# Optimization experiments

Hardware: AMD Instinct MI355X
Metric: run time of the kernel (lower is better)

Reference implementation:

```python
import jax, jax.numpy as jnp
import numpy as np

D_MODEL = 256; N_HEADS = 8; D_FFN = 1024; N_LEVELS = 4; N_POINTS = 4
HEAD_DIM = D_MODEL // N_HEADS
SHAPES = ((100, 100), (50, 50), (25, 25), (13, 13))  # static (H, W) per level
LEN_V = sum(h * w for h, w in SHAPES)  # 13294
BS = 8; NQ = 900


def layer_norm(x, g, b, eps=1e-5):
    m = x.mean(-1, keepdims=True)
    v = ((x - m) ** 2).mean(-1, keepdims=True)
    return (x - m) * jax.lax.rsqrt(v + eps) * g + b


def bilinear_sample(val, loc, H, W):
    # val: [bs, nH, H*W, hd]; loc: [bs, nq, nH, P, 2] normalized to [0,1].
    # Matches torch grid_sample(bilinear, zeros padding, align_corners=False)
    # with grid = 2*loc - 1, i.e. pixel coords x = loc_x*W - 0.5.
    bs, nq, nH, P, _ = loc.shape
    x = loc[..., 0] * W - 0.5
    y = loc[..., 1] * H - 0.5
    x0 = jnp.floor(x); y0 = jnp.floor(y)
    fx = x - x0; fy = y - y0  # grads flow to loc through fx/fy
    x0 = x0.astype(jnp.int32); y0 = y0.astype(jnp.int32)
    out = jnp.zeros((bs, nq, nH, P, HEAD_DIM), val.dtype)
    for dy, wy in ((0, 1.0 - fy), (1, fy)):
        for dx, wx in ((0, 1.0 - fx), (1, fx)):
            xi = x0 + dx; yi = y0 + dy
            valid = (xi >= 0) & (xi < W) & (yi >= 0) & (yi < H)
            idx = jnp.clip(yi, 0, H - 1) * W + jnp.clip(xi, 0, W - 1)  # [bs,nq,nH,P]
            idx = idx.transpose(0, 2, 1, 3).reshape(bs, nH, nq * P)
            g = jnp.take_along_axis(val, idx[..., None], axis=2)  # [bs,nH,nq*P,hd]
            g = g.reshape(bs, nH, nq, P, HEAD_DIM).transpose(0, 2, 1, 3, 4)
            w = (wx * wy * valid).astype(val.dtype)[..., None]
            out = out + g * w
    return out  # [bs, nq, nH, P, hd]


def setup_inputs() -> dict:
    key = jax.random.key(0)
    ks = jax.random.split(key, 16)
    d = D_MODEL
    w = lambda k, shape: (jax.random.normal(k, shape) * 0.02).astype(jnp.float32)
    z = lambda n: jnp.zeros((n,), jnp.float32)
    o = lambda n: jnp.ones((n,), jnp.float32)
    return {
        "embed": jax.random.normal(ks[0], (BS, NQ, d), jnp.float32),
        "refer_bbox": jax.random.uniform(ks[1], (BS, NQ, 4), jnp.float32),  # cxcywh in [0,1]
        "feats": jax.random.normal(ks[2], (BS, LEN_V, d), jnp.float32),
        "query_pos": jax.random.normal(ks[3], (BS, NQ, d), jnp.float32),
        "Wq": w(ks[4], (d, d)), "bq": z(d), "Wk": w(ks[5], (d, d)), "bk": z(d),
        "Wv": w(ks[6], (d, d)), "bv": z(d), "Wo": w(ks[7], (d, d)), "bo": z(d),
        "g1": o(d), "b1": z(d),
        "Wval": w(ks[8], (d, d)), "bval": z(d),
        "Woff": w(ks[9], (d, N_HEADS * N_LEVELS * N_POINTS * 2)), "boff": z(N_HEADS * N_LEVELS * N_POINTS * 2),
        "Waw": w(ks[10], (d, N_HEADS * N_LEVELS * N_POINTS)), "baw": z(N_HEADS * N_LEVELS * N_POINTS),
        "Wop": w(ks[11], (d, d)), "bop": z(d),
        "g2": o(d), "b2": z(d),
        "W1": w(ks[12], (d, D_FFN)), "bf1": z(D_FFN),
        "W2": w(ks[13], (D_FFN, d)), "bf2": z(d),
        "g3": o(d), "b3": z(d),
    }


def reference(embed, refer_bbox, feats, query_pos, Wq, bq, Wk, bk, Wv, bv, Wo, bo,
              g1, b1, Wval, bval, Woff, boff, Waw, baw, Wop, bop, g2, b2,
              W1, bf1, W2, bf2, g3, b3):
    bs, nq, d = embed.shape
    # ---- self attention (q = k = embed + query_pos, v = embed) ----
    qk_in = embed + query_pos
    q = (qk_in @ Wq + bq).reshape(bs, nq, N_HEADS, HEAD_DIM)
    k = (qk_in @ Wk + bk).reshape(bs, nq, N_HEADS, HEAD_DIM)
    v = (embed @ Wv + bv).reshape(bs, nq, N_HEADS, HEAD_DIM)
    scores = jnp.einsum('bqhd,bkhd->bhqk', q, k) * (HEAD_DIM ** -0.5)
    attn = jax.nn.softmax(scores, -1)
    sa = jnp.einsum('bhqk,bkhd->bqhd', attn, v).reshape(bs, nq, d) @ Wo + bo
    embed = layer_norm(embed + sa, g1, b1)
    # ---- MSDeformAttn cross attention ----
    query = embed + query_pos
    rb = refer_bbox[:, :, None, :]  # [bs, nq, 1, 4] (refer_bbox.unsqueeze(2))
    value = (feats @ Wval + bval).reshape(bs, LEN_V, N_HEADS, HEAD_DIM)
    off = (query @ Woff + boff).reshape(bs, nq, N_HEADS, N_LEVELS, N_POINTS, 2)
    aw = jax.nn.softmax((query @ Waw + baw).reshape(bs, nq, N_HEADS, N_LEVELS * N_POINTS), -1)
    aw = aw.reshape(bs, nq, N_HEADS, N_LEVELS, N_POINTS)
    # num_points == 4 branch: loc = cxcy + off/P * wh * 0.5
    loc = rb[:, :, None, :, None, :2] + off / N_POINTS * rb[:, :, None, :, None, 2:] * 0.5
    out = jnp.zeros((bs, nq, N_HEADS, HEAD_DIM), embed.dtype)
    start = 0
    for l, (H, W) in enumerate(SHAPES):
        val_l = value[:, start:start + H * W].transpose(0, 2, 1, 3)  # [bs,nH,HW,hd]
        s = bilinear_sample(val_l, loc[:, :, :, l], H, W)  # [bs,nq,nH,P,hd]
        out = out + (s * aw[:, :, :, l, :, None]).sum(3)
        start += H * W
    ca = out.reshape(bs, nq, d) @ Wop + bop
    embed = layer_norm(embed + ca, g2, b2)
    # ---- FFN ----
    ff = jax.nn.relu(embed @ W1 + bf1) @ W2 + bf2
    return layer_norm(embed + ff, g3, b3)
```

## Files before the change

### kernel.cpp

```cpp
#include <hip/hip_runtime.h>
#include <hip/hip_bf16.h>
#include <cstddef>

#define BS 8
#define NQ 900
#define DM 256
#define LEN_V 13294

using bf16x8 = __attribute__((ext_vector_type(8))) __bf16;
using f32x4  = __attribute__((ext_vector_type(4))) float;

__device__ __forceinline__ unsigned short f2bf(float f) {
    union { float f; unsigned int u; } v; v.f = f;
    unsigned int r = v.u + 0x7FFFu + ((v.u >> 16) & 1u);
    return (unsigned short)(r >> 16);
}
__device__ __forceinline__ float bf2f(unsigned short u) {
    union { unsigned int u; float f; } v; v.u = ((unsigned int)u) << 16;
    return v.f;
}

#define SW(r) (((r) + ((r) >> 2)) & 3)

#define FLAG_RELU 1
#define FLAG_OBF  2
#define FLAG_SWAP 4
#define FLAG_QKV  8

#define AS1(p) ((const __attribute__((address_space(1))) void*)(p))
#define AS3(p) ((__attribute__((address_space(3))) void*)(p))

#define DRAIN_DMA() do {                                   \
    __builtin_amdgcn_sched_barrier(0);                     \
    asm volatile("s_waitcnt vmcnt(0)" ::: "memory");       \
    __builtin_amdgcn_sched_barrier(0);                     \
} while (0)

struct WDesc { const float* src; unsigned short* dst; int K; int N; float scale; };
struct WPrepArgs { WDesc w[10]; };

__global__ __launch_bounds__(256) void wprep_kernel(WPrepArgs args)
{
    WDesc d = args.w[blockIdx.z];
    int k0 = blockIdx.x * 32;
    int n0 = blockIdx.y * 32;
    if (k0 >= d.K || n0 >= d.N) return;
    __shared__ unsigned short t[32][33];
    int tx = threadIdx.x & 31, ty = threadIdx.x >> 5;
    #pragma unroll
    for (int i = 0; i < 4; ++i) {
        int kk = ty + i * 8;
        t[kk][tx] = f2bf(d.src[(size_t)(k0 + kk) * d.N + n0 + tx] * d.scale);
    }
    __syncthreads();
    #pragma unroll
    for (int i = 0; i < 4; ++i) {
        int nn = ty + i * 8;
        d.dst[(size_t)(n0 + nn) * d.K + k0 + tx] = t[tx][nn];
    }
}

__global__ __launch_bounds__(256) void bias_concat_kernel(
    const float* __restrict__ bq, const float* __restrict__ bk,
    const float* __restrict__ bv, const float* __restrict__ boff,
    const float* __restrict__ baw, float* __restrict__ bqkv,
    float* __restrict__ boffaw)
{
    const float sc = 0.17677669529663687f;
    int t = blockIdx.x * 256 + threadIdx.x;
    if (t < 256)       bqkv[t] = bq[t] * sc;
    else if (t < 512)  bqkv[t] = bk[t - 256];
    else if (t < 768)  bqkv[t] = bv[t - 512];
    if (t < 256)       boffaw[t] = boff[t];
    else if (t < 384)  boffaw[t] = baw[t - 256];
}

__global__ __launch_bounds__(256) void gemm_val(
    const float* __restrict__ A, const unsigned short* __restrict__ BT,
    const float* __restrict__ bias, unsigned short* __restrict__ C,
    int M, int N, int K)
{
    __shared__ uint4 SMEM[3072];

    const int tid = threadIdx.x;
    const int lane = tid & 63;
    const int wave = tid >> 6;
    const int wm = wave >> 1;
    const int wn = wave & 1;
    const int row0 = blockIdx.y * 128;
    const int col0 = blockIdx.x * 128;

    f32x4 acc[4][4];
    #pragma unroll
    for (int i = 0; i < 4; ++i)
        #pragma unroll
        for (int j = 0; j < 4; ++j)
            acc[i][j] = {0.f, 0.f, 0.f, 0.f};

    const int lr = lane & 15;
    const int lc = lane >> 4;

    const int achunk = (lane & 7) ^ ((lane >> 3) & 7);
    const int bchunk = (lane & 3) ^ ((lane >> 2) & 3);

    auto STAGE = [&](int k0, int buf) {
        uint4* Ab = SMEM + buf * 1536;
        uint4* Bb = Ab + 1024;
        #pragma unroll
        for (int c = 0; c < 4; ++c) {
            int r = wave * 32 + c * 8 + (lane >> 3);
            int gr = row0 + r; if (gr >= M) gr = M - 1;
            const float* g = A + (size_t)gr * K + k0 + achunk * 4;
            __builtin_amdgcn_global_load_lds(AS1(g), AS3(Ab + (wave * 4 + c) * 64), 16, 0, 0);
        }
        #pragma unroll
        for (int c = 0; c < 2; ++c) {
            int r = wave * 32 + c * 16 + (lane >> 2);
            const unsigned short* g = BT + (size_t)(col0 + r) * K + k0 + bchunk * 8;
            __builtin_amdgcn_global_load_lds(AS1(g), AS3(Bb + (wave * 2 + c) * 64), 16, 0, 0);
        }
    };

    auto MSTEP = [&](int buf) {
        const float* Af = (const float*)(SMEM + buf * 1536);
        const bf16x8* Bb8 = (const bf16x8*)(SMEM + buf * 1536 + 1024);
        bf16x8 af[4], bfr[4];
        #pragma unroll
        for (int mi = 0; mi < 4; ++mi) {
            int R = wm * 64 + mi * 16 + lr;
            int s0 = (2 * lc) ^ (R & 7);
            int s1 = (2 * lc + 1) ^ (R & 7);
            f32x4 a0 = *(const f32x4*)(Af + R * 32 + s0 * 4);
            f32x4 a1 = *(const f32x4*)(Af + R * 32 + s1 * 4);
            union { unsigned short us[8]; bf16x8 v; } u;
            u.us[0] = f2bf(a0[0]); u.us[1] = f2bf(a0[1]);
            u.us[2] = f2bf(a0[2]); u.us[3] = f2bf(a0[3]);
            u.us[4] = f2bf(a1[0]); u.us[5] = f2bf(a1[1]);
            u.us[6] = f2bf(a1[2]); u.us[7] = f2bf(a1[3]);
            af[mi] = u.v;
        }
        #pragma unroll
        for (int ni = 0; ni < 4; ++ni) {
            int R = wn * 64 + ni * 16 + lr;
            bfr[ni] = Bb8[R * 4 + (lc ^ (R & 3))];
        }
        #pragma unroll
        for (int mi = 0; mi < 4; ++mi)
            #pragma unroll
            for (int ni = 0; ni < 4; ++ni)
                acc[mi][ni] = __builtin_amdgcn_mfma_f32_16x16x32_bf16(
                    af[mi], bfr[ni], acc[mi][ni], 0, 0, 0);
    };

    const int NS = K >> 5;
    STAGE(0, 0);
    DRAIN_DMA();
    __syncthreads();
    for (int s = 0; s < NS; s += 2) {
        if (s + 1 < NS) STAGE((s + 1) * 32, 1);
        MSTEP(0);
        DRAIN_DMA();
        __syncthreads();
        if (s + 2 < NS) STAGE((s + 2) * 32, 0);
        MSTEP(1);
        DRAIN_DMA();
        __syncthreads();
    }

    {
        unsigned short* RP = (unsigned short*)SMEM;
        float bval[4];
        #pragma unroll
        for (int ni = 0; ni < 4; ++ni) {
            int col = col0 + wn * 64 + ni * 16 + lr;
            bval[ni] = (col < N) ? bias[col] : 0.f;
        }
        #pragma unroll
        for (int h2 = 0; h2 < 2; ++h2) {
            __syncthreads();
            if (wm == h2) {
                #pragma unroll
                for (int ni = 0; ni < 4; ++ni) {
                    int colL = wn * 64 + ni * 16 + lr;
                    #pragma unroll
                    for (int mi = 0; mi < 4; ++mi) {
                        #pragma unroll
                        for (int rg = 0; rg < 4; ++rg) {
                            int rowL = mi * 16 + lc * 4 + rg;
                            RP[rowL * 136 + colL] = f2bf(acc[mi][ni][rg] + bval[ni]);
                        }
                    }
                }
            }
            __syncthreads();
            {
                int r = tid >> 2;
                int c = tid & 3;
                int grow = row0 + h2 * 64 + r;
                if (grow < M) {
                    #pragma unroll
                    for (int j = 0; j < 4; ++j) {
                        int gcol = col0 + c * 32 + j * 8;
                        uint4 vq = *(const uint4*)&RP[r * 136 + c * 32 + j * 8];
                        *(uint4*)(C + (size_t)grow * N + gcol) = vq;
                    }
                }
            }
        }
    }
}

#define SLOADA(B, k0) do {                                                    \
    if constexpr (ABF) {                                                      \
        const unsigned short* ap_ = Abf + (size_t)agr * K + (k0) + ah;        \
        qa##B = aok ? *(const uint4*)ap_ : z4;                                \
    } else {                                                                  \
        if (aok) {                                                            \
            const float* ap_ = Afp + (size_t)agr * K + (k0) + ah;             \
            pa##B##0 = *(const f32x4*)(ap_);                                  \
            pa##B##1 = *(const f32x4*)(ap_ + 4);                              \
            if (A2) {                                                         \
                const float* a2_ = A2 + (size_t)agr * K + (k0) + ah;          \
                pa##B##0 += *(const f32x4*)(a2_);                             \
                pa##B##1 += *(const f32x4*)(a2_ + 4);                         \
            }                                                                 \
        } else { pa##B##0 = zf4; pa##B##1 = zf4; }                            \
    }                                                                         \
    { const unsigned short* bp_ = BT + (size_t)bgr * K + (k0) + ah;           \
      pb##B = *(const uint4*)bp_; }                                           \
} while (0)

#define SSTAGE(B) do {                                                        \
    if constexpr (ABF) {                                                      \
        As4[ar * 4 + (ac ^ SW(ar))] = qa##B;                                  \
    } else {                                                                  \
        union { unsigned short us_[8]; uint4 q_; } u_;                        \
        u_.us_[0] = f2bf(pa##B##0[0]); u_.us_[1] = f2bf(pa##B##0[1]);         \
        u_.us_[2] = f2bf(pa##B##0[2]); u_.us_[3] = f2bf(pa##B##0[3]);         \
        u_.us_[4] = f2bf(pa##B##1[0]); u_.us_[5] = f2bf(pa##B##1[1]);         \
        u_.us_[6] = f2bf(pa##B##1[2]); u_.us_[7] = f2bf(pa##B##1[3]);         \
        As4[ar * 4 + (ac ^ SW(ar))] = u_.q_;                                  \
    }                                                                         \
    Bs4[ar * 4 + (ac ^ SW(ar))] = pb##B;                                      \
} while (0)

#define SMFMA() do {                                                          \
    bf16x8 af[2], bfr[2];                                                     \
    _Pragma("unroll")                                                         \
    for (int mi = 0; mi < 2; ++mi) {                                          \
        int r = wm * 32 + mi * 16 + lr;                                       \
        af[mi] = Asb[r * 4 + (lc ^ SW(r))];                                   \
    }                                                                         \
    _Pragma("unroll")                                                         \
    for (int ni = 0; ni < 2; ++ni) {                                          \
        int r = wn * 32 + ni * 16 + lr;                                       \
        bfr[ni] = Bsb[r * 4 + (lc ^ SW(r))];                                  \
    }                                                                         \
    _Pragma("unroll")                                                         \
    for (int mi = 0; mi < 2; ++mi)                                            \
        _Pragma("unroll")                                                     \
        for (int ni = 0; ni < 2; ++ni)                                        \
            acc[mi][ni] = __builtin_amdgcn_mfma_f32_16x16x32_bf16(            \
                af[mi], bfr[ni], acc[mi][ni], 0, 0, 0);                       \
} while (0)

template<int ABF>
__global__ __launch_bounds__(256) void gemm_small(
    const void* __restrict__ Ain, const float* __restrict__ A2,
    const unsigned short* __restrict__ BT, const float* __restrict__ bias,
    void* __restrict__ Cout, int M, int N, int K, int flags)
{
    __shared__ uint4 SMEM[512];
    uint4* As4 = SMEM;
    uint4* Bs4 = SMEM + 256;

    const int tid = threadIdx.x;
    const int lane = tid & 63;
    const int wave = tid >> 6;
    const int wm = wave >> 1;
    const int wn = wave & 1;
    const int row0 = (flags & FLAG_SWAP ? blockIdx.y : blockIdx.x) * 64;
    const int col0 = (flags & FLAG_SWAP ? blockIdx.x : blockIdx.y) * 64;
    if ((flags & FLAG_QKV) && col0 >= 512) A2 = nullptr;

    const float* Afp = (const float*)Ain;
    const unsigned short* Abf = (const unsigned short*)Ain;

    f32x4 acc[2][2];
    #pragma unroll
    for (int i = 0; i < 2; ++i)
        #pragma unroll
        for (int j = 0; j < 2; ++j)
            acc[i][j] = {0.f, 0.f, 0.f, 0.f};

    const int ar = tid >> 2;
    const int ac = tid & 3;
    const int ah = ac * 8;
    const int agr = row0 + ar;
    const bool aok = agr < M;
    const int bgr = col0 + ar;
    const int lr = lane & 15;
    const int lc = lane >> 4;

    const bf16x8* Asb = (const bf16x8*)As4;
    const bf16x8* Bsb = (const bf16x8*)Bs4;
    const uint4 z4 = {0u, 0u, 0u, 0u};
    const f32x4 zf4 = {0.f, 0.f, 0.f, 0.f};

    f32x4 pa00, pa01, pa10, pa11;
    uint4 qa0, qa1;
    uint4 pb0, pb1;

    const int nsteps = K >> 5;
    SLOADA(0, 0);
    for (int s = 0; s < nsteps; s += 2) {
        __syncthreads();
        SSTAGE(0);
        SLOADA(1, (s + 1 < nsteps ? (s + 1) * 32 : 0));
        __syncthreads();
        SMFMA();
        __syncthreads();
        SSTAGE(1);
        SLOADA(0, (s + 2 < nsteps ? (s + 2) * 32 : 0));
        __syncthreads();
        SMFMA();
    }

    const int relu = flags & FLAG_RELU;
    if (!(flags & FLAG_OBF)) {
        float* C = (float*)Cout;
        #pragma unroll
        for (int ni = 0; ni < 2; ++ni) {
            int col = col0 + wn * 32 + ni * 16 + lr;
            if (col >= N) continue;
            float bval = bias[col];
            #pragma unroll
            for (int mi = 0; mi < 2; ++mi) {
                #pragma unroll
                for (int rg = 0; rg < 4; ++rg) {
                    int row = row0 + wm * 32 + mi * 16 + lc * 4 + rg;
                    if (row < M) {
                        float o = acc[mi][ni][rg] + bval;
                        if (relu) o = fmaxf(o, 0.f);
                        C[(size_t)row * N + col] = o;
                    }
                }
            }
        }
    } else {
        unsigned short* RP = (unsigned short*)SMEM;
        unsigned short* C = (unsigned short*)Cout;
        float bval[2];
        #pragma unroll
        for (int ni = 0; ni < 2; ++ni) {
            int col = col0 + wn * 32 + ni * 16 + lr;
            bval[ni] = (col < N) ? bias[col] : 0.f;
        }
        #pragma unroll
        for (int h2 = 0; h2 < 2; ++h2) {
            __syncthreads();
            if (wm == h2) {
                #pragma unroll
                for (int ni = 0; ni < 2; ++ni) {
                    int colL = wn * 32 + ni * 16 + lr;
                    #pragma unroll
                    for (int mi = 0; mi < 2; ++mi) {
                        #pragma unroll
                        for (int rg = 0; rg < 4; ++rg) {
                            int rowL = mi * 16 + lc * 4 + rg;
                            float o = acc[mi][ni][rg] + bval[ni];
                            if (relu) o = fmaxf(o, 0.f);
                            RP[rowL * 72 + colL] = f2bf(o);
                        }
                    }
                }
            }
            __syncthreads();
            {
                int r = tid >> 3;
                int c = tid & 7;
                int grow = row0 + h2 * 32 + r;
                int gcol = col0 + c * 8;
                if (grow < M && gcol < N) {
                    uint4 vq = *(const uint4*)&RP[r * 72 + c * 8];
                    *(uint4*)(C + (size_t)grow * N + gcol) = vq;
                }
            }
        }
    }
}

#define QKVS 768
__global__ __launch_bounds__(256) void attn_mfma_kernel(
    const unsigned short* __restrict__ qkv, float* __restrict__ out)
{
    __shared__ uint4 Kls[64 * 4];
    __shared__ uint4 Vtls[32 * 8];

    const int tid = threadIdx.x;
    const int lane = tid & 63;
    const int wave = tid >> 6;
    const int qcol = lane & 15;
    const int g = lane >> 4;
    const int bh = blockIdx.x;
    const int h = bh & 7, b = bh >> 3;
    const int qg = blockIdx.y * 64 + wave * 16 + qcol;
    const int qc = qg < NQ ? qg : NQ - 1;

    bf16x8 qf = *(const bf16x8*)(qkv + ((size_t)(b * NQ + qc)) * QKVS + h * 32 + g * 8);

    float mrun = -3.0e38f, lrun = 0.f;
    f32x4 oacc[2];
    oacc[0] = {0.f, 0.f, 0.f, 0.f};
    oacc[1] = {0.f, 0.f, 0.f, 0.f};
    const f32x4 zacc = {0.f, 0.f, 0.f, 0.f};

    const int kidx = tid >> 2, kdc = tid & 3;
    const int vkp = tid >> 3, vdc = tid & 7;
    const bf16x8* Kb = (const bf16x8*)Kls;
    const bf16x8* Vb = (const bf16x8*)Vtls;
    unsigned int* V32 = (unsigned int*)Vtls;

    for (int jb = 0; jb < NQ; jb += 64) {
        __syncthreads();
        {
            int gk = jb + kidx;
            const uint4 z = {0u, 0u, 0u, 0u};
            uint4 kv = (gk < NQ)
                ? *(const uint4*)(qkv + ((size_t)(b * NQ + gk)) * QKVS + 256 + h * 32 + kdc * 8)
                : z;
            Kls[kidx * 4 + (kdc ^ ((kidx >> 1) & 3))] = kv;
        }
        {
            int k0g = jb + 2 * vkp;
            ushort4 a = {0, 0, 0, 0}, c = {0, 0, 0, 0};
            if (k0g < NQ)
                a = *(const ushort4*)(qkv + ((size_t)(b * NQ + k0g)) * QKVS + 512 + h * 32 + vdc * 4);
            if (k0g + 1 < NQ)
                c = *(const ushort4*)(qkv + ((size_t)(b * NQ + k0g + 1)) * QKVS + 512 + h * 32 + vdc * 4);
            unsigned int p0 = (unsigned int)a.x | ((unsigned int)c.x << 16);
            unsigned int p1 = (unsigned int)a.y | ((unsigned int)c.y << 16);
            unsigned int p2 = (unsigned int)a.z | ((unsigned int)c.z << 16);
            unsigned int p3 = (unsigned int)a.w | ((unsigned int)c.w << 16);
            int d0 = vdc * 4;
            V32[(d0+0) * 32 + ((vkp >> 2) ^ ((d0+0) & 7)) * 4 + (vkp & 3)] = p0;
            V32[(d0+1) * 32 + ((vkp >> 2) ^ ((d0+1) & 7)) * 4 + (vkp & 3)] = p1;
            V32[(d0+2) * 32 + ((vkp >> 2) ^ ((d0+2) & 7)) * 4 + (vkp & 3)] = p2;
            V32[(d0+3) * 32 + ((vkp >> 2) ^ ((d0+3) & 7)) * 4 + (vkp & 3)] = p3;
        }
        __syncthreads();

        f32x4 sacc[4];
        #pragma unroll
        for (int kt = 0; kt < 4; ++kt) {
            int key = kt * 16 + qcol;
            bf16x8 kf = Kb[key * 4 + (g ^ ((key >> 1) & 3))];
            sacc[kt] = __builtin_amdgcn_mfma_f32_16x16x32_bf16(kf, qf, zacc, 0, 0, 0);
        }
        if (jb + 64 > NQ) {
            #pragma unroll
            for (int kt = 0; kt < 4; ++kt)
                #pragma unroll
                for (int r = 0; r < 4; ++r)
                    if (jb + kt * 16 + 4 * g + r >= NQ) sacc[kt][r] = -3.0e38f;
        }

        float mloc = -3.0e38f;
        #pragma unroll
        for (int kt = 0; kt < 4; ++kt)
            #pragma unroll
            for (int r = 0; r < 4; ++r)
                mloc = fmaxf(mloc, sacc[kt][r]);
        mloc = fmaxf(mloc, __shfl_xor(mloc, 16));
        mloc = fmaxf(mloc, __shfl_xor(mloc, 32));
        float mnew = fmaxf(mrun, mloc);
        float corr = __expf(mrun - mnew);
        mrun = mnew;

        float lloc = 0.f;
        unsigned int pk2[4][2];
        #pragma unroll
        for (int kt = 0; kt < 4; ++kt) {
            float p0 = __expf(sacc[kt][0] - mnew);
            float p1 = __expf(sacc[kt][1] - mnew);
            float p2 = __expf(sacc[kt][2] - mnew);
            float p3 = __expf(sacc[kt][3] - mnew);
            lloc += p0 + p1 + p2 + p3;
            pk2[kt][0] = (unsigned int)f2bf(p0) | ((unsigned int)f2bf(p1) << 16);
            pk2[kt][1] = (unsigned int)f2bf(p2) | ((unsigned int)f2bf(p3) << 16);
        }
        lloc += __shfl_xor(lloc, 16);
        lloc += __shfl_xor(lloc, 32);
        lrun = lrun * corr + lloc;
        #pragma unroll
        for (int ni = 0; ni < 2; ++ni)
            #pragma unroll
            for (int r = 0; r < 4; ++r)
                oacc[ni][r] *= corr;

        const int s0 = qcol + 32 * (g & 1);
        const bool hi = (g >> 1) != 0;
        #pragma unroll
        for (int tp = 0; tp < 2; ++tp) {
            int A0 = (int)pk2[2 * tp][0], A1 = (int)pk2[2 * tp][1];
            int B0 = (int)pk2[2 * tp + 1][0], B1 = (int)pk2[2 * tp + 1][1];
            int a0 = __shfl(A0, s0),      a1 = __shfl(A1, s0);
            int b0 = __shfl(B0, s0),      b1 = __shfl(B1, s0);
            int a2 = __shfl(A0, s0 + 16), a3 = __shfl(A1, s0 + 16);
            int b2 = __shfl(B0, s0 + 16), b3 = __shfl(B1, s0 + 16);
            union { unsigned int u[4]; bf16x8 v8; } pf;
            pf.u[0] = hi ? (unsigned int)b0 : (unsigned int)a0;
            pf.u[1] = hi ? (unsigned int)b1 : (unsigned int)a1;
            pf.u[2] = hi ? (unsigned int)b2 : (unsigned int)a2;
            pf.u[3] = hi ? (unsigned int)b3 : (unsigned int)a3;
            #pragma unroll
            for (int ni = 0; ni < 2; ++ni) {
                int d = ni * 16 + qcol;
                bf16x8 vf = Vb[d * 8 + ((4 * tp + g) ^ (d & 7))];
                oacc[ni] = __builtin_amdgcn_mfma_f32_16x16x32_bf16(vf, pf.v8, oacc[ni], 0, 0, 0);
            }
        }
    }

    if (qg < NQ) {
        float inv = 1.f / lrun;
        float* op = out + ((size_t)(b * NQ + qg)) * DM + h * 32;
        float4 o0, o1;
        o0.x = oacc[0][0] * inv; o0.y = oacc[0][1] * inv;
        o0.z = oacc[0][2] * inv; o0.w = oacc[0][3] * inv;
        o1.x = oacc[1][0] * inv; o1.y = oacc[1][1] * inv;
        o1.z = oacc[1][2] * inv; o1.w = oacc[1][3] * inv;
        *(float4*)(op + 4 * g) = o0;
        *(float4*)(op + 16 + 4 * g) = o1;
    }
}

__global__ __launch_bounds__(256) void aw_softmax_kernel(float* __restrict__ offaw)
{
    int t = blockIdx.x * 256 + threadIdx.x;
    if (t >= BS * NQ * 8) return;
    int row = t >> 3, h = t & 7;
    float* p = offaw + (size_t)row * 384 + 256 + h * 16;
    float vals[16];
    #pragma unroll
    for (int i = 0; i < 4; ++i) {
        float4 f = *(const float4*)(p + i * 4);
        vals[4 * i + 0] = f.x; vals[4 * i + 1] = f.y;
        vals[4 * i + 2] = f.z; vals[4 * i + 3] = f.w;
    }
    float mx = vals[0];
    #pragma unroll
    for (int i = 1; i < 16; ++i) mx = fmaxf(mx, vals[i]);
    float sum = 0.f;
    #pragma unroll
    for (int i = 0; i < 16; ++i) { vals[i] = __expf(vals[i] - mx); sum += vals[i]; }
    float inv = 1.f / sum;
    #pragma unroll
    for (int i = 0; i < 4; ++i) {
        float4 f;
        f.x = vals[4 * i + 0] * inv; f.y = vals[4 * i + 1] * inv;
        f.z = vals[4 * i + 2] * inv; f.w = vals[4 * i + 3] * inv;
        *(float4*)(p + i * 4) = f;
    }
}

__global__ __launch_bounds__(256) void deform_kernel(
    const unsigned short* __restrict__ value, const float* __restrict__ offaw,
    const float* __restrict__ rbbox, float* __restrict__ dout)
{
    int t = blockIdx.x * 256 + threadIdx.x;
    if (t >= BS * NQ * 64) return;
    int c = t & 7;
    int h = (t >> 3) & 7;
    int bq = t >> 6;
    int b = bq / NQ;

    const int Hs[4]     = {100, 50, 25, 13};
    const int Wsz[4]    = {100, 50, 25, 13};
    const int Starts[4] = {0, 10000, 12500, 13125};

    float4 rb = *(const float4*)(rbbox + (size_t)bq * 4);
    const float* offp = offaw + (size_t)bq * 384 + h * 32;
    const float* awp  = offaw + (size_t)bq * 384 + 256 + h * 16;
    const unsigned short* vb = value + ((size_t)b * LEN_V) * 256 + h * 32 + c * 4;

    float4 acc = make_float4(0.f, 0.f, 0.f, 0.f);
    #pragma unroll
    for (int l = 0; l < 4; ++l) {
        const int H = Hs[l], W = Wsz[l], st = Starts[l];
        #pragma unroll
        for (int p = 0; p < 4; ++p) {
            float ox = offp[l * 8 + p * 2 + 0];
            float oy = offp[l * 8 + p * 2 + 1];
            float a_w = awp[l * 4 + p];
            float xx = (rb.x + ox * 0.125f * rb.z) * W - 0.5f;
            float yy = (rb.y + oy * 0.125f * rb.w) * H - 0.5f;
            float x0f = floorf(xx), y0f = floorf(yy);
            float fx = xx - x0f, fy = yy - y0f;
            int x0 = (int)x0f, y0 = (int)y0f;
            #pragma unroll
            for (int dy = 0; dy < 2; ++dy) {
                int yi = y0 + dy;
                float wy = dy ? fy : (1.f - fy);
                bool vy = (yi >= 0) && (yi < H);
                int yc = min(max(yi, 0), H - 1);
                #pragma unroll
                for (int dx = 0; dx < 2; ++dx) {
                    int xi = x0 + dx;
                    float wx = dx ? fx : (1.f - fx);
                    bool vx = (xi >= 0) && (xi < W);
                    int xc = min(max(xi, 0), W - 1);
                    float wgt = a_w * wy * wx * ((vx && vy) ? 1.f : 0.f);
                    ushort4 gv = *(const ushort4*)(vb + (size_t)(st + yc * W + xc) * 256);
                    acc.x += wgt * bf2f(gv.x); acc.y += wgt * bf2f(gv.y);
                    acc.z += wgt * bf2f(gv.z); acc.w += wgt * bf2f(gv.w);
                }
            }
        }
    }
    *(float4*)(dout + (size_t)bq * 256 + h * 32 + c * 4) = acc;
}

__global__ __launch_bounds__(256) void ln_kernel(
    const float* __restrict__ x, const float* __restrict__ dx,
    const float* __restrict__ g, const float* __restrict__ bt,
    float* __restrict__ out, int rows)
{
    int row = blockIdx.x * 4 + (threadIdx.x >> 6);
    if (row >= rows) return;
    int lane = threadIdx.x & 63;
    size_t base = (size_t)row * 256 + lane * 4;
    float4 xv = *(const float4*)(x + base);
    float4 dv = *(const float4*)(dx + base);
    float a0 = xv.x + dv.x, a1 = xv.y + dv.y, a2 = xv.z + dv.z, a3 = xv.w + dv.w;
    float s = a0 + a1 + a2 + a3;
    float s2 = a0 * a0 + a1 * a1 + a2 * a2 + a3 * a3;
    #pragma unroll
    for (int o = 32; o; o >>= 1) {
        s += __shfl_xor(s, o);
        s2 += __shfl_xor(s2, o);
    }
    float mean = s * (1.f / 256.f);
    float var = s2 * (1.f / 256.f) - mean * mean;
    float inv = rsqrtf(var + 1e-5f);
    float4 gv = *(const float4*)(g + lane * 4);
    float4 bv = *(const float4*)(bt + lane * 4);
    float4 r;
    r.x = (a0 - mean) * inv * gv.x + bv.x;
    r.y = (a1 - mean) * inv * gv.y + bv.y;
    r.z = (a2 - mean) * inv * gv.z + bv.z;
    r.w = (a3 - mean) * inv * gv.w + bv.w;
    *(float4*)(out + base) = r;
}

extern "C" void kernel_launch(void* const* d_in, const int* in_sizes, int n_in,
                              void* d_out, int out_size, void* d_ws, size_t ws_size,
                              hipStream_t stream)
{
    const float* embed = (const float*)d_in[0];
    const float* rbbox = (const float*)d_in[1];
    const float* feats = (const float*)d_in[2];
    const float* qpos  = (const float*)d_in[3];
    const float* Wq = (const float*)d_in[4];  const float* bq = (const float*)d_in[5];
    const float* Wk = (const float*)d_in[6];  const float* bk = (const float*)d_in[7];
    const float* Wv = (const float*)d_in[8];  const float* bv = (const float*)d_in[9];
    const float* Wo = (const float*)d_in[10]; const float* bo = (const float*)d_in[11];
    const float* g1 = (const float*)d_in[12]; const float* b1 = (const float*)d_in[13];
    const float* Wval = (const float*)d_in[14]; const float* bval = (const float*)d_in[15];
    const float* Woff = (const float*)d_in[16]; const float* boff = (const float*)d_in[17];
    const float* Waw  = (const float*)d_in[18]; const float* baw  = (const float*)d_in[19];
    const float* Wop  = (const float*)d_in[20]; const float* bop  = (const float*)d_in[21];
    const float* g2 = (const float*)d_in[22]; const float* b2 = (const float*)d_in[23];
    const float* W1 = (const float*)d_in[24]; const float* bf1 = (const float*)d_in[25];
    const float* W2 = (const float*)d_in[26]; const float* bf2 = (const float*)d_in[27];
    const float* g3 = (const float*)d_in[28]; const float* b3 = (const float*)d_in[29];

    const int M = BS * NQ;
    const int MV = BS * LEN_V;
    const size_t E = (size_t)M * DM;
    const size_t VAL = (size_t)MV * DM;

    float* ws = (float*)d_ws;
    float* valueb = ws;
    float* qkvreg = ws + VAL;
    float* attb   = qkvreg + 3 * E;
    float* e1b    = attb + E;
    unsigned short* wbase = (unsigned short*)(e1b + E);
    unsigned short* wqkv_t   = wbase;
    unsigned short* wo_t     = wbase + 196608;
    unsigned short* wval_t   = wbase + 262144;
    unsigned short* woffaw_t = wbase + 327680;
    unsigned short* wop_t    = wbase + 425984;
    unsigned short* w1_t     = wbase + 491520;
    unsigned short* w2_t     = wbase + 753664;
    float* bqkv   = (float*)(wbase + 1015808);
    float* boffaw = bqkv + 768;

    unsigned short* valuebf = (unsigned short*)valueb;
    unsigned short* qkvbf   = (unsigned short*)qkvreg;
    float* sab    = qkvreg;
    float* offawb = qkvreg + E;
    float* doutb  = attb;
    float* cab    = qkvreg;
    float* e2b    = qkvreg + 2 * E;
    unsigned short* ffhb = (unsigned short*)valueb;
    float* ffb    = attb;

    dim3 blk(256);
    auto gsS = [](int m, int n) { return dim3((n + 63) / 64, (m + 63) / 64); };

    {
        const float sc = 0.17677669529663687f;
        WPrepArgs a;
        a.w[0] = {Wq,   wqkv_t,                 256, 256,  sc};
        a.w[1] = {Wk,   wqkv_t + 256 * 256,     256, 256,  1.f};
        a.w[2] = {Wv,   wqkv_t + 512 * 256,     256, 256,  1.f};
        a.w[3] = {Wo,   wo_t,                   256, 256,  1.f};
        a.w[4] = {Wval, wval_t,                 256, 256,  1.f};
        a.w[5] = {Woff, woffaw_t,               256, 256,  1.f};
        a.w[6] = {Waw,  woffaw_t + 256 * 256,   256, 128,  1.f};
        a.w[7] = {Wop,  wop_t,                  256, 256,  1.f};
        a.w[8] = {W1,   w1_t,                   256, 1024, 1.f};
        a.w[9] = {W2,   w2_t,                   1024, 256, 1.f};
        wprep_kernel<<<dim3(32, 32, 10), blk, 0, stream>>>(a);
        bias_concat_kernel<<<dim3(3), blk, 0, stream>>>(bq, bk, bv, boff, baw, bqkv, boffaw);
    }

    gemm_small<0><<<gsS(M, 768), blk, 0, stream>>>(embed, qpos, wqkv_t, bqkv, qkvbf, M, 768, 256, FLAG_SWAP | FLAG_QKV | FLAG_OBF);
    attn_mfma_kernel<<<dim3(BS * 8, (NQ + 63) / 64), blk, 0, stream>>>(qkvbf, attb);
    gemm_small<0><<<gsS(M, 256), blk, 0, stream>>>(attb, nullptr, wo_t, bo, sab, M, 256, 256, FLAG_SWAP);
    ln_kernel<<<dim3((M + 3) / 4), blk, 0, stream>>>(embed, sab, g1, b1, e1b, M);
    gemm_val<<<dim3(2, (MV + 127) / 128), blk, 0, stream>>>(feats, wval_t, bval, valuebf, MV, 256, 256);
    gemm_small<0><<<gsS(M, 384), blk, 0, stream>>>(e1b, qpos, woffaw_t, boffaw, offawb, M, 384, 256, FLAG_SWAP);
    aw_softmax_kernel<<<dim3((BS * NQ * 8 + 255) / 256), blk, 0, stream>>>(offawb);
    deform_kernel<<<dim3((BS * NQ * 64 + 255) / 256), blk, 0, stream>>>(valuebf, offawb, rbbox, doutb);
    gemm_small<0><<<gsS(M, 256), blk, 0, stream>>>(doutb, nullptr, wop_t, bop, cab, M, 256, 256, FLAG_SWAP);
    ln_kernel<<<dim3((M + 3) / 4), blk, 0, stream>>>(e1b, cab, g2, b2, e2b, M);
    gemm_small<0><<<gsS(M, 1024), blk, 0, stream>>>(e2b, nullptr, w1_t, bf1, ffhb, M, 1024, 256, FLAG_SWAP | FLAG_RELU | FLAG_OBF);
    gemm_small<1><<<gsS(M, 256), blk, 0, stream>>>(ffhb, nullptr, w2_t, bf2, ffb, M, 256, 1024, FLAG_SWAP);
    ln_kernel<<<dim3((M + 3) / 4), blk, 0, stream>>>(e2b, ffb, g3, b3, (float*)d_out, M);
}
```

Before: 245.6 us.

## Fuse attention-weight softmax into deform kernel and relax GEMM load waits

Drops the separate softmax kernel and instead computes the 16-way attention-weight softmax inside the deformable sampling kernel, which removes one launch and one read-modify-write pass over the offset/weight buffer. Each of the 8 channel-threads per head now recomputes the same softmax, adding some redundant arithmetic. Separately, the GEMM main loop now waits with a partial vmcnt(6) instead of draining all loads, so the next stage's global loads can still be in flight while the current stage computes. It adds an extra barrier per half-step, and the fixed count of 6 assumes a specific number of outstanding loads per stage.

```diff
diff --git a/kernel.cpp b/kernel.cpp
--- a/kernel.cpp
+++ b/kernel.cpp
@@ -30,7 +30,12 @@
 #define AS1(p) ((const __attribute__((address_space(1))) void*)(p))
 #define AS3(p) ((__attribute__((address_space(3))) void*)(p))
 
-#define DRAIN_DMA() do {                                   \
+#define VMW6() do {                                        \
+    __builtin_amdgcn_sched_barrier(0);                     \
+    asm volatile("s_waitcnt vmcnt(6)" ::: "memory");       \
+    __builtin_amdgcn_sched_barrier(0);                     \
+} while (0)
+#define VMW0() do {                                        \
     __builtin_amdgcn_sched_barrier(0);                     \
     asm volatile("s_waitcnt vmcnt(0)" ::: "memory");       \
     __builtin_amdgcn_sched_barrier(0);                     \
@@ -154,18 +159,23 @@
 
     const int NS = K >> 5;
     STAGE(0, 0);
-    DRAIN_DMA();
-    __syncthreads();
     for (int s = 0; s < NS; s += 2) {
-        if (s + 1 < NS) STAGE((s + 1) * 32, 1);
+        STAGE((s + 1) * 32, 1);
+        VMW6();
+        __syncthreads();
         MSTEP(0);
-        DRAIN_DMA();
-        __syncthreads();
-        if (s + 2 < NS) STAGE((s + 2) * 32, 0);
+        __syncthreads();
+        if (s + 2 < NS) {
+            STAGE((s + 2) * 32, 0);
+            VMW6();
+        } else {
+            VMW0();
+        }
+        __syncthreads();
         MSTEP(1);
-        DRAIN_DMA();
-        __syncthreads();
-    }
+        __syncthreads();
+    }
+    VMW0();
 
     {
         unsigned short* RP = (unsigned short*)SMEM;
@@ -535,35 +545,6 @@
     }
 }
 
-__global__ __launch_bounds__(256) void aw_softmax_kernel(float* __restrict__ offaw)
-{
-    int t = blockIdx.x * 256 + threadIdx.x;
-    if (t >= BS * NQ * 8) return;
-    int row = t >> 3, h = t & 7;
-    float* p = offaw + (size_t)row * 384 + 256 + h * 16;
-    float vals[16];
-    #pragma unroll
-    for (int i = 0; i < 4; ++i) {
-        float4 f = *(const float4*)(p + i * 4);
-        vals[4 * i + 0] = f.x; vals[4 * i + 1] = f.y;
-        vals[4 * i + 2] = f.z; vals[4 * i + 3] = f.w;
-    }
-    float mx = vals[0];
-    #pragma unroll
-    for (int i = 1; i < 16; ++i) mx = fmaxf(mx, vals[i]);
-    float sum = 0.f;
-    #pragma unroll
-    for (int i = 0; i < 16; ++i) { vals[i] = __expf(vals[i] - mx); sum += vals[i]; }
-    float inv = 1.f / sum;
-    #pragma unroll
-    for (int i = 0; i < 4; ++i) {
-        float4 f;
-        f.x = vals[4 * i + 0] * inv; f.y = vals[4 * i + 1] * inv;
-        f.z = vals[4 * i + 2] * inv; f.w = vals[4 * i + 3] * inv;
-        *(float4*)(p + i * 4) = f;
-    }
-}
-
 __global__ __launch_bounds__(256) void deform_kernel(
     const unsigned short* __restrict__ value, const float* __restrict__ offaw,
     const float* __restrict__ rbbox, float* __restrict__ dout)
@@ -584,6 +565,20 @@
     const float* awp  = offaw + (size_t)bq * 384 + 256 + h * 16;
     const unsigned short* vb = value + ((size_t)b * LEN_V) * 256 + h * 32 + c * 4;
 
+    float awv[16];
+    #pragma unroll
+    for (int i = 0; i < 4; ++i) {
+        float4 f = *(const float4*)(awp + i * 4);
+        awv[4*i+0] = f.x; awv[4*i+1] = f.y; awv[4*i+2] = f.z; awv[4*i+3] = f.w;
+    }
+    float mx = awv[0];
+    #pragma unroll
+    for (int i = 1; i < 16; ++i) mx = fmaxf(mx, awv[i]);
+    float ssum = 0.f;
+    #pragma unroll
+    for (int i = 0; i < 16; ++i) { awv[i] = __expf(awv[i] - mx); ssum += awv[i]; }
+    float sinv = 1.f / ssum;
+
     float4 acc = make_float4(0.f, 0.f, 0.f, 0.f);
     #pragma unroll
     for (int l = 0; l < 4; ++l) {
@@ -592,7 +587,7 @@
         for (int p = 0; p < 4; ++p) {
             float ox = offp[l * 8 + p * 2 + 0];
             float oy = offp[l * 8 + p * 2 + 1];
-            float a_w = awp[l * 4 + p];
+            float a_w = awv[l * 4 + p] * sinv;
             float xx = (rb.x + ox * 0.125f * rb.z) * W - 0.5f;
             float yy = (rb.y + oy * 0.125f * rb.w) * H - 0.5f;
             float x0f = floorf(xx), y0f = floorf(yy);
@@ -732,7 +727,6 @@
     ln_kernel<<<dim3((M + 3) / 4), blk, 0, stream>>>(embed, sab, g1, b1, e1b, M);
     gemm_val<<<dim3(2, (MV + 127) / 128), blk, 0, stream>>>(feats, wval_t, bval, valuebf, MV, 256, 256);
     gemm_small<0><<<gsS(M, 384), blk, 0, stream>>>(e1b, qpos, woffaw_t, boffaw, offawb, M, 384, 256, FLAG_SWAP);
-    aw_softmax_kernel<<<dim3((BS * NQ * 8 + 255) / 256), blk, 0, stream>>>(offawb);
     deform_kernel<<<dim3((BS * NQ * 64 + 255) / 256), blk, 0, stream>>>(valuebf, offawb, rbbox, doutb);
     gemm_small<0><<<gsS(M, 256), blk, 0, stream>>>(doutb, nullptr, wop_t, bop, cab, M, 256, 256, FLAG_SWAP);
     ln_kernel<<<dim3((M + 3) / 4), blk, 0, stream>>>(e1b, cab, g2, b2, e2b, M);
```

Result: no change. 243.0 us (-1.1%).
